# Performance work log

Hardware: AMD Instinct MI355X
Metric: run time of the kernel (lower is better)

## Reference

```python
import jax, jax.numpy as jnp
import numpy as np

# FlowNetC correlation config (matches init_kwargs)
PAD = 20          # pad_size
KERNEL = 1        # kernel_size (kernel_radius = 0)
MAX_DISP = 20     # max_displacement
STRIDE1 = 1       # output stride
STRIDE2 = 2       # displacement stride
RAD = MAX_DISP // STRIDE2   # neighborhood_grid_radius = 10 -> 21x21 = 441 displacements


def setup_inputs() -> dict:
    key = jax.random.key(0)
    k1, k2 = jax.random.split(key)
    B, C, H, W = 4, 256, 64, 96
    return {
        "input1": jax.random.normal(k1, (B, C, H, W), dtype=jnp.float32),
        "input2": jax.random.normal(k2, (B, C, H, W), dtype=jnp.float32),
    }


def reference(input1, input2):
    # input1, input2: [B, C, H, W]
    # Output: [B, (2*RAD+1)**2, H, W]  (pad_size == max_displacement, stride1 == 1,
    # kernel_size == 1 => output spatial size equals input spatial size).
    B, C, H, W = input1.shape
    p2 = jnp.pad(input2, ((0, 0), (0, 0), (PAD, PAD), (PAD, PAD)))
    norm = jnp.asarray(KERNEL * KERNEL * C, dtype=input1.dtype)
    outs = []
    # Fixed, small displacement grid (21x21): static slicing per displacement
    # avoids materializing a [441, B, C, H, W] intermediate.
    for dy in range(-RAD, RAD + 1):
        oy = PAD + dy * STRIDE2
        for dx in range(-RAD, RAD + 1):
            ox = PAD + dx * STRIDE2
            shifted = p2[:, :, oy:oy + H, ox:ox + W]        # [B, C, H, W]
            outs.append(jnp.sum(input1 * shifted, axis=1))  # [B, H, W]
    corr = jnp.stack(outs, axis=1) / norm                    # [B, 441, H, W]
    return corr
```

## Files before the change

kernel.cpp:

```cpp
#include <hip/hip_runtime.h>


typedef short bf16x8 __attribute__((ext_vector_type(8)));
typedef float f32x4  __attribute__((ext_vector_type(4)));

#define PLANE 24576
#define BP    260
#define ST    40

__device__ __forceinline__ short f2bf(float f) {
    union { float f; unsigned u; } x; x.f = f;
    const unsigned u = x.u;
    return (short)((u + 0x7fffu + ((u >> 16) & 1u)) >> 16);
}

__global__ __launch_bounds__(256)
void corr_prepass(const float* __restrict__ in1, const float* __restrict__ in2,
                  short* __restrict__ dstA, short* __restrict__ dstB) {
    const int bid = blockIdx.x;
    const int sel = bid >> 8;
    const int r   = bid & 255;
    const int b   = r >> 6;
    const int yt  = (r >> 3) & 7;
    const int ct  = r & 7;
    const int c0 = ct * 32, y0 = yt * 8;
    const float* src = sel ? in2 : in1;
    short* dst = sel ? dstB : dstA;

    __shared__ __align__(16) short T[768 * ST];
    const int tid = threadIdx.x;

#pragma unroll
    for (int it = 0; it < 3; ++it) {
        const int d = it * 256 + tid;
        const int g = d / 192;
        const int f = d - g * 192;
        float4 v[8];
#pragma unroll
        for (int j = 0; j < 8; ++j) {
            const int c = c0 + g * 8 + j;
            v[j] = *(const float4*)(src + ((size_t)(b * 256 + c) * 64 + y0) * 96 + 4 * f);
        }
        bf16x8 w0, w1, w2, w3;
#pragma unroll
        for (int j = 0; j < 8; ++j) {
            w0[j] = f2bf(v[j].x); w1[j] = f2bf(v[j].y);
            w2[j] = f2bf(v[j].z); w3[j] = f2bf(v[j].w);
        }
        const int perm = ((g ^ (f & 3)) * 8);
        const int base = 4 * f * ST + perm;
        *(bf16x8*)&T[base]          = w0;
        *(bf16x8*)&T[base + ST]     = w1;
        *(bf16x8*)&T[base + 2*ST]   = w2;
        *(bf16x8*)&T[base + 3*ST]   = w3;
    }
    __syncthreads();

#pragma unroll
    for (int it = 0; it < 12; ++it) {
        const int D  = it * 256 + tid;
        const int Rl = D >> 2, gp = D & 3;
        const int yy  = Rl / 96;
        const int rl  = Rl - yy * 96;
        const int par = rl / 48;
        const int col = rl - par * 48;
        const int x   = 2 * col + par;
        const int xx  = yy * 96 + x;
        const int perm = ((gp ^ ((xx >> 2) & 3)) * 8);
        const bf16x8 w = *(const bf16x8*)&T[xx * ST + perm];
        const size_t Rg = (size_t)(b * 64 + y0 + yy) * 96 + par * 48 + col;
        *(bf16x8*)(dst + Rg * 256 + c0 + gp * 8) = w;
    }
}

__global__ __launch_bounds__(256, 2)
void corr_mfma(const short* __restrict__ Ag, const short* __restrict__ Bg,
               float* __restrict__ out) {
    const int bid = blockIdx.x;
    const int pg  = bid >> 8;
    const int by2 = bid & 255;
    const int b = by2 >> 6, y2 = by2 & 63;
    const int p0 = pg ? 6 : 0, p1 = pg ? 11 : 6;

    const int tid  = threadIdx.x;
    const int lane = tid & 63, w = tid >> 6;
    const int par  = w & 1, slot = w >> 1;
    const int n    = lane & 15, q = lane >> 4;

    __shared__ __align__(16) short Bsh[96 * BP];
    __shared__ __align__(16) float scr[2][21 * 97];

    {
        const short* src = Bg + (size_t)by2 * PLANE;
#pragma unroll
        for (int it = 0; it < 12; ++it) {
            const int j = it * 256 + tid;
            *(bf16x8*)&Bsh[(j >> 5) * BP + (j & 31) * 8] = *(const bf16x8*)(src + j * 8);
        }
    }
    __syncthreads();

    const bool v0 = (n >= 10), v3 = (n < 10);
    const int  r0c = v0 ? (n - 10) : 0;
    const int  r3c = v3 ? (n + 38) : 0;
    const short* Bp = &Bsh[par * 48 * BP];

    for (int p = p0; p < p1; ++p) {
        const int dyp = 2 * p + slot;
        const int y   = y2 + 20 - 2 * dyp;
        const bool live = (dyp < 21) && (y >= 0) && (y < 64);

        f32x4 acc[9];
#pragma unroll
        for (int t2 = 0; t2 < 9; ++t2) acc[t2] = (f32x4)0.0f;

        if (live) {
            const short* Ap = Ag + ((size_t)(b * 64 + y) * 96 + par * 48) * 256;
            bf16x8 af[3][8];
#pragma unroll
            for (int ks = 0; ks < 8; ++ks)
#pragma unroll
                for (int Xi = 0; Xi < 3; ++Xi)
                    af[Xi][ks] = *(const bf16x8*)(Ap + (Xi * 16 + n) * 256 + ks * 32 + q * 8);

#pragma unroll
            for (int ks = 0; ks < 8; ++ks) {
                const int ko = ks * 32 + q * 8;
                bf16x8 b0 = *(const bf16x8*)&Bp[r0c * BP + ko];     if (!v0) b0 = 0;
                bf16x8 b1 = *(const bf16x8*)&Bp[(n + 6)  * BP + ko];
                bf16x8 b2 = *(const bf16x8*)&Bp[(n + 22) * BP + ko];
                bf16x8 b3 = *(const bf16x8*)&Bp[r3c * BP + ko];     if (!v3) b3 = 0;
                acc[0] = __builtin_amdgcn_mfma_f32_16x16x32_bf16(af[0][ks], b0, acc[0], 0, 0, 0);
                acc[1] = __builtin_amdgcn_mfma_f32_16x16x32_bf16(af[0][ks], b1, acc[1], 0, 0, 0);
                acc[2] = __builtin_amdgcn_mfma_f32_16x16x32_bf16(af[0][ks], b2, acc[2], 0, 0, 0);
                acc[3] = __builtin_amdgcn_mfma_f32_16x16x32_bf16(af[1][ks], b1, acc[3], 0, 0, 0);
                acc[4] = __builtin_amdgcn_mfma_f32_16x16x32_bf16(af[1][ks], b2, acc[4], 0, 0, 0);
                acc[5] = __builtin_amdgcn_mfma_f32_16x16x32_bf16(af[1][ks], b3, acc[5], 0, 0, 0);
                acc[6] = __builtin_amdgcn_mfma_f32_16x16x32_bf16(af[2][ks], b2, acc[6], 0, 0, 0);
                acc[7] = __builtin_amdgcn_mfma_f32_16x16x32_bf16(af[2][ks], b3, acc[7], 0, 0, 0);
            }

            float* sc = scr[slot];
            const int mb = q * 4;
#pragma unroll
            for (int t2 = 0; t2 < 9; ++t2) {
                const int Xi = (t2 < 3) ? 0 : (t2 < 6 ? 1 : 2);
                constexpr int UJ[9] = {0, 1, 2, 1, 2, 3, 2, 3, 4};
                const int ub = UJ[t2] * 16;
#pragma unroll
                for (int rr = 0; rr < 4; ++rr) {
                    const int xe = Xi * 16 + mb + rr;
                    const int k  = ub + n - xe;
                    if ((unsigned)k < 21u)
                        sc[k * 97 + 2 * xe + par] = acc[t2][rr];
                }
            }
        }
        __syncthreads();

#pragma unroll
        for (int it = 0; it < 16; ++it) {
            const int e = it * 256 + tid;
            if (e < 4032) {
                const int s  = e / 2016;
                const int f  = e - s * 2016;
                const int k  = f / 96;
                const int x  = f - k * 96;
                const int dd = 2 * p + s;
                const int yd = y2 + 20 - 2 * dd;
                if (dd < 21 && yd >= 0 && yd < 64)
                    out[((size_t)(b * 441 + dd * 21 + k) * 64 + yd) * 96 + x] =
                        scr[s][k * 97 + x] * (1.0f / 256.0f);
            }
        }
        __syncthreads();
    }
}

extern "C" void kernel_launch(void* const* d_in, const int* in_sizes, int n_in,
                              void* d_out, int out_size, void* d_ws, size_t ws_size,
                              hipStream_t stream) {
    const float* in1 = (const float*)d_in[0];
    const float* in2 = (const float*)d_in[1];
    float* out = (float*)d_out;

    short* Ag = (short*)d_ws;
    short* Bg = Ag + (size_t)256 * PLANE;

    corr_prepass<<<dim3(512), dim3(256), 0, stream>>>(in1, in2, Ag, Bg);
    corr_mfma<<<dim3(512), dim3(256), 0, stream>>>(Ag, Bg, out);
}
```

Before: 150.1 us.

## Prefetch next A fragments during MFMA, split work finer, widen prepass tiles

The MFMA kernel now loads the A fragments for the next displacement row while the current row's MFMAs and scatter run, so global-load latency overlaps compute. The grid doubles to 1024 blocks with 3 row-pairs each instead of 6/5, improving balance at the cost of reloading the B tile more often. The prepass switches to 64-channel tiles with a new LDS layout and swizzle and launches half as many blocks. Holding the prefetch buffer across iterations raises register pressure under the 2-wave occupancy bound.

```diff
diff --git a/kernel.cpp b/kernel.cpp
--- a/kernel.cpp
+++ b/kernel.cpp
@@ -6,7 +6,6 @@
 
 #define PLANE 24576
 #define BP    260
-#define ST    40
 
 __device__ __forceinline__ short f2bf(float f) {
     union { float f; unsigned u; } x; x.f = f;
@@ -18,28 +17,30 @@
 void corr_prepass(const float* __restrict__ in1, const float* __restrict__ in2,
                   short* __restrict__ dstA, short* __restrict__ dstB) {
     const int bid = blockIdx.x;
-    const int sel = bid >> 8;
-    const int r   = bid & 255;
-    const int b   = r >> 6;
-    const int yt  = (r >> 3) & 7;
-    const int ct  = r & 7;
-    const int c0 = ct * 32, y0 = yt * 8;
+    const int sel = bid >> 7;
+    const int r   = bid & 127;
+    const int b   = r >> 5;
+    const int yt  = (r >> 2) & 7;
+    const int ct  = r & 3;
+    const int c0 = ct * 64, y0 = yt * 8;
     const float* src = sel ? in2 : in1;
     short* dst = sel ? dstB : dstA;
 
-    __shared__ __align__(16) short T[768 * ST];
+    __shared__ __align__(16) short T[6144 * 8];
     const int tid = threadIdx.x;
 
 #pragma unroll
-    for (int it = 0; it < 3; ++it) {
+    for (int it = 0; it < 6; ++it) {
         const int d = it * 256 + tid;
         const int g = d / 192;
         const int f = d - g * 192;
+        const int yy = f / 24;
+        const int xf = 4 * (f - yy * 24);
         float4 v[8];
 #pragma unroll
         for (int j = 0; j < 8; ++j) {
             const int c = c0 + g * 8 + j;
-            v[j] = *(const float4*)(src + ((size_t)(b * 256 + c) * 64 + y0) * 96 + 4 * f);
+            v[j] = *(const float4*)(src + ((size_t)(b * 256 + c) * 64 + y0 + yy) * 96 + xf);
         }
         bf16x8 w0, w1, w2, w3;
 #pragma unroll
@@ -47,29 +48,27 @@
             w0[j] = f2bf(v[j].x); w1[j] = f2bf(v[j].y);
             w2[j] = f2bf(v[j].z); w3[j] = f2bf(v[j].w);
         }
-        const int perm = ((g ^ (f & 3)) * 8);
-        const int base = 4 * f * ST + perm;
-        *(bf16x8*)&T[base]          = w0;
-        *(bf16x8*)&T[base + ST]     = w1;
-        *(bf16x8*)&T[base + 2*ST]   = w2;
-        *(bf16x8*)&T[base + 3*ST]   = w3;
+        const int pc = g ^ (f & 7);
+        const int a0 = (4 * f) * 64 + pc * 8;
+        *(bf16x8*)&T[a0]       = w0;
+        *(bf16x8*)&T[a0 + 64]  = w1;
+        *(bf16x8*)&T[a0 + 128] = w2;
+        *(bf16x8*)&T[a0 + 192] = w3;
     }
     __syncthreads();
 
 #pragma unroll
-    for (int it = 0; it < 12; ++it) {
+    for (int it = 0; it < 24; ++it) {
         const int D  = it * 256 + tid;
-        const int Rl = D >> 2, gp = D & 3;
-        const int yy  = Rl / 96;
-        const int rl  = Rl - yy * 96;
-        const int par = rl / 48;
-        const int col = rl - par * 48;
-        const int x   = 2 * col + par;
-        const int xx  = yy * 96 + x;
-        const int perm = ((gp ^ ((xx >> 2) & 3)) * 8);
-        const bf16x8 w = *(const bf16x8*)&T[xx * ST + perm];
-        const size_t Rg = (size_t)(b * 64 + y0 + yy) * 96 + par * 48 + col;
-        *(bf16x8*)(dst + Rg * 256 + c0 + gp * 8) = w;
+        const int xx = D >> 3;
+        const int pc = D & 7;
+        const int cx = pc ^ ((xx >> 2) & 7);
+        const bf16x8 w = *(const bf16x8*)&T[D * 8];
+        const int yy = xx / 96;
+        const int x  = xx - yy * 96;
+        const int rl = (x & 1) * 48 + (x >> 1);
+        const size_t Rg = (size_t)(b * 64 + y0 + yy) * 96 + rl;
+        *(bf16x8*)(dst + Rg * 256 + c0 + cx * 8) = w;
     }
 }
 
@@ -80,7 +79,8 @@
     const int pg  = bid >> 8;
     const int by2 = bid & 255;
     const int b = by2 >> 6, y2 = by2 & 63;
-    const int p0 = pg ? 6 : 0, p1 = pg ? 11 : 6;
+    const int p0 = pg * 3;
+    const int p1 = (p0 + 3 < 11) ? (p0 + 3) : 11;
 
     const int tid  = threadIdx.x;
     const int lane = tid & 63, w = tid >> 6;
@@ -105,6 +105,20 @@
     const int  r3c = v3 ? (n + 38) : 0;
     const short* Bp = &Bsh[par * 48 * BP];
 
+    bf16x8 af[3][8];
+    {
+        const int dyp = 2 * p0 + slot;
+        const int yy  = y2 + 20 - 2 * dyp;
+        if (dyp < 21 && yy >= 0 && yy < 64) {
+            const short* Ap = Ag + ((size_t)(b * 64 + yy) * 96 + par * 48) * 256;
+#pragma unroll
+            for (int ks = 0; ks < 8; ++ks)
+#pragma unroll
+                for (int Xi = 0; Xi < 3; ++Xi)
+                    af[Xi][ks] = *(const bf16x8*)(Ap + (Xi * 16 + n) * 256 + ks * 32 + q * 8);
+        }
+    }
+
     for (int p = p0; p < p1; ++p) {
         const int dyp = 2 * p + slot;
         const int y   = y2 + 20 - 2 * dyp;
@@ -115,14 +129,6 @@
         for (int t2 = 0; t2 < 9; ++t2) acc[t2] = (f32x4)0.0f;
 
         if (live) {
-            const short* Ap = Ag + ((size_t)(b * 64 + y) * 96 + par * 48) * 256;
-            bf16x8 af[3][8];
-#pragma unroll
-            for (int ks = 0; ks < 8; ++ks)
-#pragma unroll
-                for (int Xi = 0; Xi < 3; ++Xi)
-                    af[Xi][ks] = *(const bf16x8*)(Ap + (Xi * 16 + n) * 256 + ks * 32 + q * 8);
-
 #pragma unroll
             for (int ks = 0; ks < 8; ++ks) {
                 const int ko = ks * 32 + q * 8;
@@ -139,7 +145,22 @@
                 acc[6] = __builtin_amdgcn_mfma_f32_16x16x32_bf16(af[2][ks], b2, acc[6], 0, 0, 0);
                 acc[7] = __builtin_amdgcn_mfma_f32_16x16x32_bf16(af[2][ks], b3, acc[7], 0, 0, 0);
             }
-
+        }
+
+        if (p + 1 < p1) {
+            const int dn = 2 * (p + 1) + slot;
+            const int yn = y2 + 20 - 2 * dn;
+            if (dn < 21 && yn >= 0 && yn < 64) {
+                const short* Ap = Ag + ((size_t)(b * 64 + yn) * 96 + par * 48) * 256;
+#pragma unroll
+                for (int ks = 0; ks < 8; ++ks)
+#pragma unroll
+                    for (int Xi = 0; Xi < 3; ++Xi)
+                        af[Xi][ks] = *(const bf16x8*)(Ap + (Xi * 16 + n) * 256 + ks * 32 + q * 8);
+            }
+        }
+
+        if (live) {
             float* sc = scr[slot];
             const int mb = q * 4;
 #pragma unroll
@@ -187,6 +208,6 @@
     short* Ag = (short*)d_ws;
     short* Bg = Ag + (size_t)256 * PLANE;
 
-    corr_prepass<<<dim3(512), dim3(256), 0, stream>>>(in1, in2, Ag, Bg);
-    corr_mfma<<<dim3(512), dim3(256), 0, stream>>>(Ag, Bg, out);
-}
+    corr_prepass<<<dim3(256), dim3(256), 0, stream>>>(in1, in2, Ag, Bg);
+    corr_mfma<<<dim3(1024), dim3(256), 0, stream>>>(Ag, Bg, out);
+}
```

New measurement: 215.8 us. 1.44x slower.

## Fuse bf16 conversion prepass into correlation MFMA kernel, reading fp32 inputs directly

Applied to the files above, without the earlier changes.

Drops the separate prepass kernel that converted both inputs to channel-last bf16 in workspace. The main kernel now loads its input2 row in fp32, converts it and transposes it into shared memory itself. Input1 fragments are gathered straight from fp32 NCHW with scalar strided loads, one element per channel. This saves a kernel launch and the workspace round trip, but the A loads become uncoalesced scalar reads repeated across blocks and displacement steps, so global traffic may rise.

```diff
diff --git a/kernel.cpp b/kernel.cpp
--- a/kernel.cpp
+++ b/kernel.cpp
@@ -4,9 +4,7 @@
 typedef short bf16x8 __attribute__((ext_vector_type(8)));
 typedef float f32x4  __attribute__((ext_vector_type(4)));
 
-#define PLANE 24576
-#define BP    260
-#define ST    40
+#define BP 260
 
 __device__ __forceinline__ short f2bf(float f) {
     union { float f; unsigned u; } x; x.f = f;
@@ -14,68 +12,9 @@
     return (short)((u + 0x7fffu + ((u >> 16) & 1u)) >> 16);
 }
 
-__global__ __launch_bounds__(256)
-void corr_prepass(const float* __restrict__ in1, const float* __restrict__ in2,
-                  short* __restrict__ dstA, short* __restrict__ dstB) {
-    const int bid = blockIdx.x;
-    const int sel = bid >> 8;
-    const int r   = bid & 255;
-    const int b   = r >> 6;
-    const int yt  = (r >> 3) & 7;
-    const int ct  = r & 7;
-    const int c0 = ct * 32, y0 = yt * 8;
-    const float* src = sel ? in2 : in1;
-    short* dst = sel ? dstB : dstA;
-
-    __shared__ __align__(16) short T[768 * ST];
-    const int tid = threadIdx.x;
-
-#pragma unroll
-    for (int it = 0; it < 3; ++it) {
-        const int d = it * 256 + tid;
-        const int g = d / 192;
-        const int f = d - g * 192;
-        float4 v[8];
-#pragma unroll
-        for (int j = 0; j < 8; ++j) {
-            const int c = c0 + g * 8 + j;
-            v[j] = *(const float4*)(src + ((size_t)(b * 256 + c) * 64 + y0) * 96 + 4 * f);
-        }
-        bf16x8 w0, w1, w2, w3;
-#pragma unroll
-        for (int j = 0; j < 8; ++j) {
-            w0[j] = f2bf(v[j].x); w1[j] = f2bf(v[j].y);
-            w2[j] = f2bf(v[j].z); w3[j] = f2bf(v[j].w);
-        }
-        const int perm = ((g ^ (f & 3)) * 8);
-        const int base = 4 * f * ST + perm;
-        *(bf16x8*)&T[base]          = w0;
-        *(bf16x8*)&T[base + ST]     = w1;
-        *(bf16x8*)&T[base + 2*ST]   = w2;
-        *(bf16x8*)&T[base + 3*ST]   = w3;
-    }
-    __syncthreads();
-
-#pragma unroll
-    for (int it = 0; it < 12; ++it) {
-        const int D  = it * 256 + tid;
-        const int Rl = D >> 2, gp = D & 3;
-        const int yy  = Rl / 96;
-        const int rl  = Rl - yy * 96;
-        const int par = rl / 48;
-        const int col = rl - par * 48;
-        const int x   = 2 * col + par;
-        const int xx  = yy * 96 + x;
-        const int perm = ((gp ^ ((xx >> 2) & 3)) * 8);
-        const bf16x8 w = *(const bf16x8*)&T[xx * ST + perm];
-        const size_t Rg = (size_t)(b * 64 + y0 + yy) * 96 + par * 48 + col;
-        *(bf16x8*)(dst + Rg * 256 + c0 + gp * 8) = w;
-    }
-}
-
 __global__ __launch_bounds__(256, 2)
-void corr_mfma(const short* __restrict__ Ag, const short* __restrict__ Bg,
-               float* __restrict__ out) {
+void corr_one(const float* __restrict__ in1, const float* __restrict__ in2,
+              float* __restrict__ out) {
     const int bid = blockIdx.x;
     const int pg  = bid >> 8;
     const int by2 = bid & 255;
@@ -90,13 +29,25 @@
     __shared__ __align__(16) short Bsh[96 * BP];
     __shared__ __align__(16) float scr[2][21 * 97];
 
-    {
-        const short* src = Bg + (size_t)by2 * PLANE;
 #pragma unroll
-        for (int it = 0; it < 12; ++it) {
-            const int j = it * 256 + tid;
-            *(bf16x8*)&Bsh[(j >> 5) * BP + (j & 31) * 8] = *(const bf16x8*)(src + j * 8);
+    for (int it = 0; it < 3; ++it) {
+        const int d = it * 256 + tid;
+        const int g = d / 24;
+        const int f = d - g * 24;
+        float4 v[8];
+#pragma unroll
+        for (int j = 0; j < 8; ++j)
+            v[j] = *(const float4*)(in2 + ((size_t)(b * 256 + g * 8 + j) * 64 + y2) * 96 + 4 * f);
+        bf16x8 w0, w1, w2, w3;
+#pragma unroll
+        for (int j = 0; j < 8; ++j) {
+            w0[j] = f2bf(v[j].x); w1[j] = f2bf(v[j].y);
+            w2[j] = f2bf(v[j].z); w3[j] = f2bf(v[j].w);
         }
+        *(bf16x8*)&Bsh[(2 * f)          * BP + g * 8] = w0;
+        *(bf16x8*)&Bsh[(48 + 2 * f)     * BP + g * 8] = w1;
+        *(bf16x8*)&Bsh[(2 * f + 1)      * BP + g * 8] = w2;
+        *(bf16x8*)&Bsh[(48 + 2 * f + 1) * BP + g * 8] = w3;
     }
     __syncthreads();
 
@@ -104,6 +55,8 @@
     const int  r0c = v0 ? (n - 10) : 0;
     const int  r3c = v3 ? (n + 38) : 0;
     const short* Bp = &Bsh[par * 48 * BP];
+
+    const int xoff = 2 * n + par;
 
     for (int p = p0; p < p1; ++p) {
         const int dyp = 2 * p + slot;
@@ -115,29 +68,31 @@
         for (int t2 = 0; t2 < 9; ++t2) acc[t2] = (f32x4)0.0f;
 
         if (live) {
-            const short* Ap = Ag + ((size_t)(b * 64 + y) * 96 + par * 48) * 256;
-            bf16x8 af[3][8];
+            const float* Arow = in1 + ((size_t)(b * 256) * 64 + y) * 96 + xoff;
+
+#pragma unroll 2
+            for (int ks = 0; ks < 8; ++ks) {
+                bf16x8 a0v, a1v, a2v;
 #pragma unroll
-            for (int ks = 0; ks < 8; ++ks)
-#pragma unroll
-                for (int Xi = 0; Xi < 3; ++Xi)
-                    af[Xi][ks] = *(const bf16x8*)(Ap + (Xi * 16 + n) * 256 + ks * 32 + q * 8);
-
-#pragma unroll
-            for (int ks = 0; ks < 8; ++ks) {
+                for (int j = 0; j < 8; ++j) {
+                    const float* Ac = Arow + (size_t)(ks * 32 + q * 8 + j) * 6144;
+                    a0v[j] = f2bf(Ac[0]);
+                    a1v[j] = f2bf(Ac[32]);
+                    a2v[j] = f2bf(Ac[64]);
+                }
                 const int ko = ks * 32 + q * 8;
                 bf16x8 b0 = *(const bf16x8*)&Bp[r0c * BP + ko];     if (!v0) b0 = 0;
                 bf16x8 b1 = *(const bf16x8*)&Bp[(n + 6)  * BP + ko];
                 bf16x8 b2 = *(const bf16x8*)&Bp[(n + 22) * BP + ko];
                 bf16x8 b3 = *(const bf16x8*)&Bp[r3c * BP + ko];     if (!v3) b3 = 0;
-                acc[0] = __builtin_amdgcn_mfma_f32_16x16x32_bf16(af[0][ks], b0, acc[0], 0, 0, 0);
-                acc[1] = __builtin_amdgcn_mfma_f32_16x16x32_bf16(af[0][ks], b1, acc[1], 0, 0, 0);
-                acc[2] = __builtin_amdgcn_mfma_f32_16x16x32_bf16(af[0][ks], b2, acc[2], 0, 0, 0);
-                acc[3] = __builtin_amdgcn_mfma_f32_16x16x32_bf16(af[1][ks], b1, acc[3], 0, 0, 0);
-                acc[4] = __builtin_amdgcn_mfma_f32_16x16x32_bf16(af[1][ks], b2, acc[4], 0, 0, 0);
-                acc[5] = __builtin_amdgcn_mfma_f32_16x16x32_bf16(af[1][ks], b3, acc[5], 0, 0, 0);
-                acc[6] = __builtin_amdgcn_mfma_f32_16x16x32_bf16(af[2][ks], b2, acc[6], 0, 0, 0);
-                acc[7] = __builtin_amdgcn_mfma_f32_16x16x32_bf16(af[2][ks], b3, acc[7], 0, 0, 0);
+                acc[0] = __builtin_amdgcn_mfma_f32_16x16x32_bf16(a0v, b0, acc[0], 0, 0, 0);
+                acc[1] = __builtin_amdgcn_mfma_f32_16x16x32_bf16(a0v, b1, acc[1], 0, 0, 0);
+                acc[2] = __builtin_amdgcn_mfma_f32_16x16x32_bf16(a0v, b2, acc[2], 0, 0, 0);
+                acc[3] = __builtin_amdgcn_mfma_f32_16x16x32_bf16(a1v, b1, acc[3], 0, 0, 0);
+                acc[4] = __builtin_amdgcn_mfma_f32_16x16x32_bf16(a1v, b2, acc[4], 0, 0, 0);
+                acc[5] = __builtin_amdgcn_mfma_f32_16x16x32_bf16(a1v, b3, acc[5], 0, 0, 0);
+                acc[6] = __builtin_amdgcn_mfma_f32_16x16x32_bf16(a2v, b2, acc[6], 0, 0, 0);
+                acc[7] = __builtin_amdgcn_mfma_f32_16x16x32_bf16(a2v, b3, acc[7], 0, 0, 0);
             }
 
             float* sc = scr[slot];
@@ -184,9 +139,5 @@
     const float* in2 = (const float*)d_in[1];
     float* out = (float*)d_out;
 
-    short* Ag = (short*)d_ws;
-    short* Bg = Ag + (size_t)256 * PLANE;
-
-    corr_prepass<<<dim3(512), dim3(256), 0, stream>>>(in1, in2, Ag, Bg);
-    corr_mfma<<<dim3(512), dim3(256), 0, stream>>>(Ag, Bg, out);
+    corr_one<<<dim3(512), dim3(256), 0, stream>>>(in1, in2, out);
 }
```

Result: slower. 178.7 us (+19.1%).
